# Kernel tuning notes

Measured on AMD Instinct MI355X. Metric: run time of the kernel, lower is better.

Reference implementation:

```python
import jax, jax.numpy as jnp
import numpy as np

ROUTING = 3
N_VERTEX = 32
D_CAP = 16
MULT_D = 64
B = 64
T_DIMS = {"text": 128, "audio": 512, "video": 256, "frames": 256}


def _xavier(key, shape):
    # torch xavier_normal_ on (T, n, MULT_d, d_c): receptive = MULT_d*d_c
    T, n, j, d = shape
    recep = j * d
    std = np.sqrt(2.0 / (n * recep + T * recep))
    return jax.random.normal(key, shape, dtype=jnp.float32) * std


def setup_inputs() -> dict:
    key = jax.random.key(0)
    ks = jax.random.split(key, 8)
    inp = {}
    for i, (name, T) in enumerate(T_DIMS.items()):
        inp[name] = jax.random.normal(ks[i], (B, T, MULT_D), dtype=jnp.float32)
    wnames = ["W_tpc", "W_apc", "W_vpc", "W_fpc"]
    for i, (name, (_, T)) in enumerate(zip(wnames, T_DIMS.items())):
        inp[name] = _xavier(ks[4 + i], (T, N_VERTEX, MULT_D, D_CAP))
    return inp


def _route(pri, routing):
    # pri: [B, T, n, d_c]; routing uses detached (stop-gradient) capsules
    pri_sg = jax.lax.stop_gradient(pri)
    Bn, T, n, d = pri.shape
    b = jnp.zeros((Bn, T, n), dtype=pri.dtype)
    for _ in range(routing):
        rc = jax.nn.softmax(b, axis=2)                      # [B, T, n]
        v = jnp.tanh(jnp.einsum('btnd,btn->bnd', pri_sg, rc))
        b = b + jnp.einsum('bnd,btnd->btn', v, pri_sg)      # agreement update
    rc = jnp.softmax(b, axis=2) if False else jax.nn.softmax(b, axis=2)
    # final vertex uses non-detached capsules with last routing coefficients
    return jnp.tanh(jnp.einsum('btnd,btn->bnd', pri, rc))


def reference(text, audio, video, frames, W_tpc, W_apc, W_vpc, W_fpc):
    outs = []
    for x, W in ((text, W_tpc), (audio, W_apc), (video, W_vpc), (frames, W_fpc)):
        pri = jnp.einsum('btj,tnjd->btnd', x, W)  # primary capsules [B,T,n,d_c]
        outs.append(_route(pri, ROUTING))
    return tuple(outs)
```

## Files before the change

### kernel.cpp

```cpp
#include <hip/hip_runtime.h>


typedef __attribute__((ext_vector_type(8))) short short8;
typedef __attribute__((ext_vector_type(4))) float floatx4;

static __device__ __forceinline__ unsigned short f2bf(float f) {
  union { float f; unsigned int i; } v;
  v.f = f;
  unsigned int x = v.i;
  return (unsigned short)((x + 0x7fffu + ((x >> 16) & 1u)) >> 16);
}

__global__ __launch_bounds__(256, 3) void pri_kernel(
    const float* __restrict__ x0, const float* __restrict__ x1,
    const float* __restrict__ x2, const float* __restrict__ x3,
    const float* __restrict__ w0, const float* __restrict__ w1,
    const float* __restrict__ w2, const float* __restrict__ w3,
    unsigned short* __restrict__ priAll) {
  __shared__ unsigned short wb[256 * 72];
  __shared__ unsigned short sc[4][16][136];

  int blk = blockIdx.x;
  int tid = threadIdx.x;

  int pair = blk >> 1, half = blk & 1;
  const float* x;
  const float* W;
  unsigned short* priT;
  int T, t0;
  if (pair < 64)       { x = x0; W = w0; priT = priAll;               T = 128; t0 = 2 * pair; }
  else if (pair < 320) { x = x1; W = w1; priT = priAll + 4194304ull;  T = 512; t0 = 2 * (pair - 64); }
  else if (pair < 448) { x = x2; W = w2; priT = priAll + 20971520ull; T = 256; t0 = 2 * (pair - 320); }
  else                 { x = x3; W = w3; priT = priAll + 29360128ull; T = 256; t0 = 2 * (pair - 448); }
  unsigned short* priT0 = priT + (size_t)t0 * 32768;
  unsigned short* priT1 = priT + (size_t)(t0 + 1) * 32768;

  int lane = tid & 63, mt = tid >> 6;
  int m = lane & 15, q = lane >> 4;

  floatx4 xv[8];
  {
    const float* xrow = x + ((size_t)(mt * 16 + m) * T + t0) * 64;
#pragma unroll
    for (int tt = 0; tt < 2; ++tt)
#pragma unroll
      for (int s = 0; s < 2; ++s) {
        const floatx4* xp = (const floatx4*)(xrow + tt * 64 + s * 32 + q * 8);
        xv[tt * 4 + s * 2]     = __builtin_nontemporal_load(xp);
        xv[tt * 4 + s * 2 + 1] = __builtin_nontemporal_load(xp + 1);
      }
  }

  floatx4 wra[8], wrb[8];
  {
    const floatx4* Wf = (const floatx4*)(W + (size_t)t0 * 32768);
#pragma unroll
    for (int it = 0; it < 8; ++it) {
      int idx = it * 256 + tid;
      int nl = idx >> 7, jp = (idx >> 2) & 31, dq = idx & 3;
      int ng = half * 16 + nl;
      wra[it] = __builtin_nontemporal_load(Wf + ng * 256 + (2 * jp) * 4 + dq);
      wrb[it] = __builtin_nontemporal_load(Wf + ng * 256 + (2 * jp + 1) * 4 + dq);
    }
  }

  short8 afrag[2][2];
#pragma unroll
  for (int tt = 0; tt < 2; ++tt)
#pragma unroll
    for (int s = 0; s < 2; ++s) {
      floatx4 u0 = xv[tt * 4 + s * 2], u1 = xv[tt * 4 + s * 2 + 1];
      short8 a;
      a[0] = (short)f2bf(u0[0]); a[1] = (short)f2bf(u0[1]);
      a[2] = (short)f2bf(u0[2]); a[3] = (short)f2bf(u0[3]);
      a[4] = (short)f2bf(u1[0]); a[5] = (short)f2bf(u1[1]);
      a[6] = (short)f2bf(u1[2]); a[7] = (short)f2bf(u1[3]);
      afrag[tt][s] = a;
    }

  unsigned int* wb32 = (unsigned int*)wb;

#pragma unroll
  for (int it = 0; it < 8; ++it) {
    int idx = it * 256 + tid;
    int nl = idx >> 7, jp = (idx >> 2) & 31, dq = idx & 3;
    int rbase = nl * 16 + dq * 4;
#pragma unroll
    for (int k = 0; k < 4; ++k) {
      unsigned int dw = (unsigned int)f2bf(wra[it][k]) | ((unsigned int)f2bf(wrb[it][k]) << 16);
      wb32[(rbase + k) * 36 + jp] = dw;
    }
  }
  __syncthreads();

  {
    const floatx4* Wf = (const floatx4*)(W + (size_t)(t0 + 1) * 32768);
#pragma unroll
    for (int it = 0; it < 8; ++it) {
      int idx = it * 256 + tid;
      int nl = idx >> 7, jp = (idx >> 2) & 31, dq = idx & 3;
      int ng = half * 16 + nl;
      wra[it] = __builtin_nontemporal_load(Wf + ng * 256 + (2 * jp) * 4 + dq);
      wrb[it] = __builtin_nontemporal_load(Wf + ng * 256 + (2 * jp + 1) * 4 + dq);
    }
  }

  auto compute_t = [&](const short8& a0, const short8& a1, unsigned short* dst) {
    for (int g2 = 0; g2 < 2; ++g2) {
#pragma unroll
      for (int k = 0; k < 8; ++k) {
        int nt = g2 * 8 + k;
        const short8* b0p = (const short8*)&wb[(nt * 16 + m) * 72 + q * 8];
        const short8* b1p = (const short8*)&wb[(nt * 16 + m) * 72 + 32 + q * 8];
        short8 bf0 = *b0p, bf1 = *b1p;
        floatx4 acc = {0.f, 0.f, 0.f, 0.f};
        acc = __builtin_amdgcn_mfma_f32_16x16x32_bf16(a0, bf0, acc, 0, 0, 0);
        acc = __builtin_amdgcn_mfma_f32_16x16x32_bf16(a1, bf1, acc, 0, 0, 0);
#pragma unroll
        for (int reg = 0; reg < 4; ++reg)
          sc[mt][q * 4 + reg][k * 16 + m] = f2bf(acc[reg]);
      }
#pragma unroll
      for (int i = 0; i < 4; ++i) {
        int bl = (lane >> 4) + i * 4;
        int sh = (lane & 15) * 8;
        short8 v = *(const short8*)&sc[mt][bl][sh];
        *(short8*)(dst + (size_t)(mt * 16 + bl) * 512 + half * 256 + g2 * 128 + sh) = v;
      }
    }
  };

  compute_t(afrag[0][0], afrag[0][1], priT0);
  __syncthreads();

#pragma unroll
  for (int it = 0; it < 8; ++it) {
    int idx = it * 256 + tid;
    int nl = idx >> 7, jp = (idx >> 2) & 31, dq = idx & 3;
    int rbase = nl * 16 + dq * 4;
#pragma unroll
    for (int k = 0; k < 4; ++k) {
      unsigned int dw = (unsigned int)f2bf(wra[it][k]) | ((unsigned int)f2bf(wrb[it][k]) << 16);
      wb32[(rbase + k) * 36 + jp] = dw;
    }
  }
  __syncthreads();

  compute_t(afrag[1][0], afrag[1][1], priT1);
}

__global__ __launch_bounds__(1024) void route_kernel(
    const unsigned short* __restrict__ priAll, float* __restrict__ out) {
  __shared__ float Sl[32][640];
  __shared__ float Vc_s[544];

  int blk = blockIdx.x;
  int mod = blk & 3, b = blk >> 2;
  size_t poff; int T;
  if (mod == 0)      { poff = 0ull;         T = 128; }
  else if (mod == 1) { poff = 4194304ull;   T = 512; }
  else if (mod == 2) { poff = 20971520ull;  T = 256; }
  else               { poff = 29360128ull;  T = 256; }

  const unsigned short* priM = priAll + poff + (size_t)b * 512;

  int tid = threadIdx.x;
  int n = tid & 31, g = tid >> 5;
  int nbase = n * 17;

  if (tid < 544) Vc_s[tid] = 0.f;
  __syncthreads();

  int iters = T >> 5;

  for (int pass = 0; pass < 4; ++pass) {
    float Vc[16];
#pragma unroll
    for (int d = 0; d < 16; ++d) Vc[d] = Vc_s[nbase + d];

    float acc[16];
#pragma unroll
    for (int d = 0; d < 16; ++d) acc[d] = 0.f;

    const uint4* pr = (const uint4*)(priM + (size_t)g * 32768 + n * 16);
    uint4 ca = pr[0], cb = pr[1];

    for (int it = 0; it < iters; ++it) {
      uint4 na, nb;
      bool more = (it + 1 < iters);
      if (more) { na = pr[131072]; nb = pr[131073]; }

      float p[16];
      {
        unsigned int wds[8] = {ca.x, ca.y, ca.z, ca.w, cb.x, cb.y, cb.z, cb.w};
#pragma unroll
        for (int k = 0; k < 8; ++k) {
          union { unsigned int u; float f; } lo, hi;
          lo.u = wds[k] << 16;
          hi.u = wds[k] & 0xffff0000u;
          p[2 * k] = lo.f;
          p[2 * k + 1] = hi.f;
        }
      }
      float logit = 0.f;
#pragma unroll
      for (int d = 0; d < 16; ++d) logit += p[d] * Vc[d];
      float e = __expf(logit);
      float s = e;
#pragma unroll
      for (int o = 16; o >= 1; o >>= 1) s += __shfl_xor(s, o, 32);
      float rc = e / s;
#pragma unroll
      for (int d = 0; d < 16; ++d) acc[d] += rc * p[d];

      if (more) { ca = na; cb = nb; pr += 131072; }
    }

#pragma unroll
    for (int d = 0; d < 16; ++d) Sl[g][nbase + d] = acc[d];
    __syncthreads();

    if (tid < 512) {
      int nn = tid >> 4, dd = tid & 15;
      int idx = nn * 17 + dd;
      float s = 0.f;
#pragma unroll
      for (int gg = 0; gg < 32; ++gg) s += Sl[gg][idx];
      float v = tanhf(s);
      if (pass == 3) out[(size_t)(mod * 64 + b) * 512 + tid] = v;
      else Vc_s[idx] += v;
    }
    __syncthreads();
  }
}

extern "C" void kernel_launch(void* const* d_in, const int* in_sizes, int n_in,
                              void* d_out, int out_size, void* d_ws, size_t ws_size,
                              hipStream_t stream) {
  const float* x0 = (const float*)d_in[0];
  const float* x1 = (const float*)d_in[1];
  const float* x2 = (const float*)d_in[2];
  const float* x3 = (const float*)d_in[3];
  const float* w0 = (const float*)d_in[4];
  const float* w1 = (const float*)d_in[5];
  const float* w2 = (const float*)d_in[6];
  const float* w3 = (const float*)d_in[7];

  unsigned short* pri = (unsigned short*)d_ws;

  pri_kernel<<<1152, 256, 0, stream>>>(x0, x1, x2, x3, w0, w1, w2, w3, pri);
  route_kernel<<<256, 1024, 0, stream>>>(pri, (float*)d_out);
}
```

Baseline: 241.8 us.

## Store primary capsules batch-major and deepen route prefetch to two steps

The intermediate primary-capsule buffer switches from [T][B][n*d] to [B][T][n*d] order. Each route block, which handles one batch element, now streams a contiguous region instead of 1 KB chunks spread across the whole tensor. The pri kernel's stores become strided by T*512 per batch row in exchange. The route loop also prefetches two iterations ahead instead of one, to hide more global load latency at the cost of extra registers.

```diff
diff --git a/kernel.cpp b/kernel.cpp
--- a/kernel.cpp
+++ b/kernel.cpp
@@ -26,14 +26,13 @@
   int pair = blk >> 1, half = blk & 1;
   const float* x;
   const float* W;
-  unsigned short* priT;
+  unsigned short* priM;
   int T, t0;
-  if (pair < 64)       { x = x0; W = w0; priT = priAll;               T = 128; t0 = 2 * pair; }
-  else if (pair < 320) { x = x1; W = w1; priT = priAll + 4194304ull;  T = 512; t0 = 2 * (pair - 64); }
-  else if (pair < 448) { x = x2; W = w2; priT = priAll + 20971520ull; T = 256; t0 = 2 * (pair - 320); }
-  else                 { x = x3; W = w3; priT = priAll + 29360128ull; T = 256; t0 = 2 * (pair - 448); }
-  unsigned short* priT0 = priT + (size_t)t0 * 32768;
-  unsigned short* priT1 = priT + (size_t)(t0 + 1) * 32768;
+  if (pair < 64)       { x = x0; W = w0; priM = priAll;               T = 128; t0 = 2 * pair; }
+  else if (pair < 320) { x = x1; W = w1; priM = priAll + 4194304ull;  T = 512; t0 = 2 * (pair - 64); }
+  else if (pair < 448) { x = x2; W = w2; priM = priAll + 20971520ull; T = 256; t0 = 2 * (pair - 320); }
+  else                 { x = x3; W = w3; priM = priAll + 29360128ull; T = 256; t0 = 2 * (pair - 448); }
+  size_t TS = (size_t)T * 512;
 
   int lane = tid & 63, mt = tid >> 6;
   int m = lane & 15, q = lane >> 4;
@@ -105,7 +104,8 @@
     }
   }
 
-  auto compute_t = [&](const short8& a0, const short8& a1, unsigned short* dst) {
+  auto compute_t = [&](const short8& a0, const short8& a1, int t) {
+    unsigned short* dst = priM + (size_t)t * 512 + half * 256;
     for (int g2 = 0; g2 < 2; ++g2) {
 #pragma unroll
       for (int k = 0; k < 8; ++k) {
@@ -125,12 +125,12 @@
         int bl = (lane >> 4) + i * 4;
         int sh = (lane & 15) * 8;
         short8 v = *(const short8*)&sc[mt][bl][sh];
-        *(short8*)(dst + (size_t)(mt * 16 + bl) * 512 + half * 256 + g2 * 128 + sh) = v;
+        *(short8*)(dst + (size_t)(mt * 16 + bl) * TS + g2 * 128 + sh) = v;
       }
     }
   };
 
-  compute_t(afrag[0][0], afrag[0][1], priT0);
+  compute_t(afrag[0][0], afrag[0][1], t0);
   __syncthreads();
 
 #pragma unroll
@@ -146,7 +146,7 @@
   }
   __syncthreads();
 
-  compute_t(afrag[1][0], afrag[1][1], priT1);
+  compute_t(afrag[1][0], afrag[1][1], t0 + 1);
 }
 
 __global__ __launch_bounds__(1024) void route_kernel(
@@ -162,7 +162,7 @@
   else if (mod == 2) { poff = 20971520ull;  T = 256; }
   else               { poff = 29360128ull;  T = 256; }
 
-  const unsigned short* priM = priAll + poff + (size_t)b * 512;
+  const unsigned short* priM = priAll + poff + (size_t)b * T * 512;
 
   int tid = threadIdx.x;
   int n = tid & 31, g = tid >> 5;
@@ -182,13 +182,14 @@
 #pragma unroll
     for (int d = 0; d < 16; ++d) acc[d] = 0.f;
 
-    const uint4* pr = (const uint4*)(priM + (size_t)g * 32768 + n * 16);
+    const uint4* pr = (const uint4*)(priM + (size_t)g * 512 + n * 16);
     uint4 ca = pr[0], cb = pr[1];
+    uint4 na = pr[2048], nb = pr[2049];
+    uint4 fa = {}, fb = {};
 
     for (int it = 0; it < iters; ++it) {
-      uint4 na, nb;
-      bool more = (it + 1 < iters);
-      if (more) { na = pr[131072]; nb = pr[131073]; }
+      bool more2 = (it + 2 < iters);
+      if (more2) { fa = pr[4096]; fb = pr[4097]; }
 
       float p[16];
       {
@@ -213,7 +214,8 @@
 #pragma unroll
       for (int d = 0; d < 16; ++d) acc[d] += rc * p[d];
 
-      if (more) { ca = na; cb = nb; pr += 131072; }
+      ca = na; cb = nb; na = fa; nb = fb;
+      pr += 2048;
     }
 
 #pragma unroll
```

Result: no change. 244.0 us (+0.9%).
